# Kernel tuning notes

Hardware: AMD Instinct MI355X
Metric: run time of the kernel (lower is better)

Reference implementation:

```python
import jax, jax.numpy as jnp
import numpy as np

B, T, D = 1, 2048, 2048
N_HEADS, N_KV = 32, 8
HD = D // N_HEADS          # 64
G = N_HEADS // N_KV        # 4 query heads per kv head


def setup_inputs() -> dict:
    key = jax.random.key(0)
    ks = jax.random.split(key, 8)
    x = jax.random.normal(ks[0], (B, T, D), dtype=jnp.float32)
    cos = jax.random.uniform(ks[1], (1, 1, T, HD), dtype=jnp.float32)
    sin = jax.random.uniform(ks[2], (1, 1, T, HD), dtype=jnp.float32)
    attention_mask = jnp.ones((B, T), dtype=jnp.int32)
    s = 1.0 / np.sqrt(D)
    Wq = jax.random.normal(ks[3], (D, D), dtype=jnp.float32) * s
    Wk = jax.random.normal(ks[4], (D, N_KV * HD), dtype=jnp.float32) * s
    Wv = jax.random.normal(ks[5], (D, N_KV * HD), dtype=jnp.float32) * s
    Wo = jax.random.normal(ks[6], (D, D), dtype=jnp.float32) * s
    return {"x": x, "cos": cos, "sin": sin, "attention_mask": attention_mask,
            "Wq": Wq, "Wk": Wk, "Wv": Wv, "Wo": Wo}


def rotate_half(t):
    t1, t2 = jnp.split(t, 2, axis=-1)
    return jnp.concatenate((-t2, t1), axis=-1)


def reference(x, cos, sin, attention_mask, Wq, Wk, Wv, Wo):
    b, t, d = x.shape
    # projections (Linear, no bias); weights stored as [in, out]
    q = (x @ Wq).reshape(b, t, N_HEADS, HD).transpose(0, 2, 1, 3)   # [B,H,T,hd]
    k = (x @ Wk).reshape(b, t, N_KV, HD).transpose(0, 2, 1, 3)      # [B,Kv,T,hd]
    v = (x @ Wv).reshape(b, t, N_KV, HD).transpose(0, 2, 1, 3)      # [B,Kv,T,hd]
    # RoPE
    q = q * cos + rotate_half(q) * sin
    k = k * cos + rotate_half(k) * sin
    # GQA without materializing repeated KV: group query heads by kv head
    qg = q.reshape(b, N_KV, G, t, HD)                               # [B,Kv,G,T,hd]
    scale = 1.0 / jnp.sqrt(jnp.asarray(HD, dtype=x.dtype))
    scores = jnp.einsum('bkgqd,bkcd->bkgqc', qg, k) * scale          # [B,Kv,G,T,T]
    neg = jnp.finfo(x.dtype).min
    # padding mask: (1 - mask) * finfo.min, broadcast over heads/query pos
    pad = (1.0 - attention_mask.astype(x.dtype)) * neg               # [B,T]
    scores = scores + pad[:, None, None, None, :]
    # causal mask
    causal = jnp.tril(jnp.ones((t, t), dtype=bool))
    scores = jnp.where(causal[None, None, None, :, :], scores, neg)
    p = jax.nn.softmax(scores, axis=-1)
    y = jnp.einsum('bkgqc,bkcd->bkgqd', p, v)                        # [B,Kv,G,T,hd]
    y = y.reshape(b, N_HEADS, t, HD).transpose(0, 2, 1, 3).reshape(b, t, d)
    return y @ Wo
```

## Files before the change

### kernel.cpp

```cpp
#include <hip/hip_runtime.h>
#include <hip/hip_bf16.h>
#include <math.h>

typedef __attribute__((ext_vector_type(4))) float f32x4;
typedef __attribute__((ext_vector_type(8))) short bf16x8;
typedef __attribute__((ext_vector_type(4))) short bf16x4;
typedef unsigned short u16;
typedef unsigned int u32;


__device__ __forceinline__ float exp2fast(float x) {
    return __builtin_amdgcn_exp2f(x);
}
__device__ __forceinline__ u16 f2bf(float f) {
    return __builtin_bit_cast(u16, __float2bfloat16(f));
}
__device__ __forceinline__ float bf2f(u16 h) {
    return __builtin_bit_cast(float, ((u32)h) << 16);
}

#define GLL16(gsrc, ldst) __builtin_amdgcn_global_load_lds( \
    (const __attribute__((address_space(1))) u32*)(gsrc),   \
    (__attribute__((address_space(3))) u32*)(ldst), 16, 0, 0)

__device__ __forceinline__ void tconv_body(const float* __restrict__ in, u16* __restrict__ out,
                                           int R, int C, int bx, int by,
                                           float (*tile)[33], int tx, int ty) {
    int c0 = bx * 32, r0 = by * 32;
    #pragma unroll
    for (int i = 0; i < 4; ++i)
        tile[ty + i * 8][tx] = in[(size_t)(r0 + ty + i * 8) * C + c0 + tx];
    __syncthreads();
    #pragma unroll
    for (int i = 0; i < 4; ++i)
        out[(size_t)(c0 + ty + i * 8) * R + r0 + tx] = f2bf(tile[tx][ty + i * 8]);
}

__global__ void k_prep(const float* __restrict__ x, u16* __restrict__ xb,
                       const float* __restrict__ Wq, const float* __restrict__ Wk,
                       const float* __restrict__ Wv, const float* __restrict__ Wo,
                       u16* __restrict__ Wt, u16* __restrict__ WoT) {
    __shared__ float tile[32][33];
    const int r = blockIdx.x;
    const int tx = threadIdx.x, ty = threadIdx.y;
    if (r < 4096) {
        int tid = ty * 32 + tx;
        int base = (r * 256 + tid) * 4;
        float4 v = *(const float4*)(x + base);
        ushort4 o;
        o.x = f2bf(v.x); o.y = f2bf(v.y); o.z = f2bf(v.z); o.w = f2bf(v.w);
        *(ushort4*)(xb + base) = o;
    } else if (r < 8192) {
        int rr = r - 4096;  tconv_body(Wq, Wt, 2048, 2048, rr & 63, rr >> 6, tile, tx, ty);
    } else if (r < 9216) {
        int rr = r - 8192;  tconv_body(Wk, Wt + (size_t)2048 * 2048, 2048, 512, rr & 15, rr >> 4, tile, tx, ty);
    } else if (r < 10240) {
        int rr = r - 9216;  tconv_body(Wv, Wt + (size_t)2560 * 2048, 2048, 512, rr & 15, rr >> 4, tile, tx, ty);
    } else {
        int rr = r - 10240; tconv_body(Wo, WoT, 2048, 2048, rr & 63, rr >> 6, tile, tx, ty);
    }
}

__global__ void k_vprep(const u16* __restrict__ QKV,
                        const int* __restrict__ maskp, float* __restrict__ padf,
                        u16* __restrict__ Vt, int* __restrict__ padAny) {
    __shared__ u16 tile[32][34];
    const int r = blockIdx.x;
    const int tx = threadIdx.x, ty = threadIdx.y;
    if (r < 1024) {
        int c0 = (r & 15) * 32, r0 = (r >> 4) * 32;
        const u16* in = QKV + 2560;
        #pragma unroll
        for (int i = 0; i < 4; ++i)
            tile[ty + i * 8][tx] = in[(size_t)(r0 + ty + i * 8) * 3072 + c0 + tx];
        __syncthreads();
        int kv = r0 + tx;
        int kvp = (kv & ~63) + (((kv >> 5) & 1) << 5) + (((kv >> 2) & 3) << 3)
                + (((kv >> 4) & 1) << 2) + (kv & 3);
        #pragma unroll
        for (int i = 0; i < 4; ++i)
            Vt[(size_t)(c0 + ty + i * 8) * 2048 + kvp] = tile[tx][ty + i * 8];
    } else if (r < 1032) {
        int tid = ty * 32 + tx;
        int t = (r - 1024) * 256 + tid;
        padf[t] = maskp[t] ? 0.0f : -3.4028235e38f;
    } else {
        int t64 = r - 1032;
        int tid = ty * 32 + tx;
        if (tid < 64) {
            bool anypad = (maskp[t64 * 64 + tid] == 0);
            unsigned long long b = __ballot(anypad);
            if (tid == 0) padAny[t64] = (b != 0ULL) ? 1 : 0;
        }
    }
}

template<int OUTF32, int ROPE>
__global__ __launch_bounds__(256) void k_gemm(const u16* __restrict__ A, int lda,
                                              const u16* __restrict__ Bt,
                                              void* __restrict__ Cv,
                                              int M, int N, int K,
                                              const float* __restrict__ cosp,
                                              const float* __restrict__ sinp) {
    __shared__ u16 As[2][64 * 64];
    __shared__ u16 Bs[2][128 * 64];
    const int tid = threadIdx.x;
    const int w = tid >> 6, lane = tid & 63;
    const int wr = w & 1, wc = w >> 1;
    const int g = lane >> 4, l15 = lane & 15;
    const int m0 = blockIdx.y * 64, n0 = blockIdx.x * 128;

    f32x4 acc[2][4] = {};

    const u16* gA[2];
    const u16* gB[4];
    #pragma unroll
    for (int i = 0; i < 2; ++i) {
        int c = tid + i * 256;
        int rr = c >> 3, kc = (c & 7) ^ (rr & 7);
        gA[i] = A + (size_t)(m0 + rr) * lda + kc * 8;
    }
    #pragma unroll
    for (int i = 0; i < 4; ++i) {
        int c = tid + i * 256;
        int rr = c >> 3, kc = (c & 7) ^ (rr & 7);
        gB[i] = Bt + (size_t)(n0 + rr) * K + kc * 8;
    }

    auto stageAB = [&](int b, int k0) {
        #pragma unroll
        for (int i = 0; i < 2; ++i)
            GLL16(gA[i] + k0, &As[b][(tid + i * 256) * 8]);
        #pragma unroll
        for (int i = 0; i < 4; ++i)
            GLL16(gB[i] + k0, &Bs[b][(tid + i * 256) * 8]);
    };

    stageAB(0, 0);
    __syncthreads();
    int buf = 0;

    for (int k0 = 0; k0 < K; k0 += 64) {
        int kn = k0 + 64;
        if (kn < K) stageAB(buf ^ 1, kn);

        bf16x8 af[2][2], bfr[4][2];
        #pragma unroll
        for (int mt = 0; mt < 2; ++mt) {
            int row = wr * 32 + mt * 16 + l15;
            int rb = row * 64;
            #pragma unroll
            for (int kk = 0; kk < 2; ++kk) {
                int slot = (kk * 4 + g) ^ (row & 7);
                af[mt][kk] = *(const bf16x8*)&As[buf][rb + slot * 8];
            }
        }
        #pragma unroll
        for (int nt = 0; nt < 4; ++nt) {
            int row = wc * 64 + nt * 16 + l15;
            int rb = row * 64;
            #pragma unroll
            for (int kk = 0; kk < 2; ++kk) {
                int slot = (kk * 4 + g) ^ (row & 7);
                bfr[nt][kk] = *(const bf16x8*)&Bs[buf][rb + slot * 8];
            }
        }
        #pragma unroll
        for (int mt = 0; mt < 2; ++mt)
            #pragma unroll
            for (int nt = 0; nt < 4; ++nt) {
                acc[mt][nt] = __builtin_amdgcn_mfma_f32_16x16x32_bf16(af[mt][0], bfr[nt][0], acc[mt][nt], 0, 0, 0);
                acc[mt][nt] = __builtin_amdgcn_mfma_f32_16x16x32_bf16(af[mt][1], bfr[nt][1], acc[mt][nt], 0, 0, 0);
            }
        __syncthreads();
        buf ^= 1;
    }

    if (ROPE && n0 < 2560) {
        const float sc = (n0 < 2048) ? 0.18033688f : 1.0f;
        #pragma unroll
        for (int mt = 0; mt < 2; ++mt) {
            #pragma unroll
            for (int rr = 0; rr < 4; ++rr) {
                int t = m0 + wr * 32 + mt * 16 + g * 4 + rr;
                #pragma unroll
                for (int nt = 0; nt < 2; ++nt) {
                    int jh = nt * 16 + l15;
                    float c1 = cosp[t * 64 + jh],      s1 = sinp[t * 64 + jh];
                    float c2 = cosp[t * 64 + jh + 32], s2 = sinp[t * 64 + jh + 32];
                    float a = acc[mt][nt][rr], b = acc[mt][nt + 2][rr];
                    acc[mt][nt][rr]     = (a * c1 - b * s1) * sc;
                    acc[mt][nt + 2][rr] = (b * c2 + a * s2) * sc;
                }
            }
        }
    }

    #pragma unroll
    for (int mt = 0; mt < 2; ++mt) {
        #pragma unroll
        for (int nt = 0; nt < 4; ++nt) {
            int mrow = m0 + wr * 32 + mt * 16 + g * 4;
            int ncol = n0 + wc * 64 + nt * 16 + l15;
            #pragma unroll
            for (int rr = 0; rr < 4; ++rr) {
                float v = acc[mt][nt][rr];
                if (OUTF32) ((float*)Cv)[(size_t)(mrow + rr) * N + ncol] = v;
                else        ((u16*)Cv)[(size_t)(mrow + rr) * N + ncol] = f2bf(v);
            }
        }
    }
}

__global__ __launch_bounds__(512) void k_attn(const u16* __restrict__ QKV,
                                              const u16* __restrict__ VtG,
                                              const float* __restrict__ padf,
                                              const int* __restrict__ padAny,
                                              u16* __restrict__ Ob) {
    __shared__ u16 Ks[2][64 * 64];
    __shared__ u16 Vs[2][64 * 64];
    const int kvh = blockIdx.y;
    const int x = (int)blockIdx.x;
    const int tid = threadIdx.x;
    const int w = tid >> 6, lane = tid & 63;
    const int g = lane >> 4, l15 = lane & 15;
    const int h = kvh * 4 + (w & 3);
    const int q0w = (w >> 2) == 0 ? x * 16 : (127 - x) * 16;
    const int q = q0w + l15;
    const int myfull = q0w >> 6;
    const int iters = (((127 - x) * 16) >> 6) + 1;
    const bf16x8 ones8 = {(short)0x3F80, (short)0x3F80, (short)0x3F80, (short)0x3F80,
                          (short)0x3F80, (short)0x3F80, (short)0x3F80, (short)0x3F80};

    const u16* qrow = QKV + (size_t)q * 3072 + h * 64;
    bf16x8 qf0 = *(const bf16x8*)(qrow + g * 8);
    bf16x8 qf1 = *(const bf16x8*)(qrow + 32 + g * 8);

    f32x4 oacc[4] = {};
    float m_run = -1e30f, l_run = 0.0f;

    auto stage = [&](int b, int kv0) {
        int p = tid;
        int rr = p >> 3, c = p & 7;
        int cs = c ^ (rr & 7);
        GLL16(QKV + (size_t)(kv0 + rr) * 3072 + 2048 + kvh * 64 + cs * 8, &Ks[b][p * 8]);
        GLL16(VtG + (size_t)(kvh * 64 + rr) * 2048 + kv0 + cs * 8, &Vs[b][p * 8]);
    };

    stage(0, 0);
    __syncthreads();
    int buf = 0;

    for (int t = 0; t < iters; ++t) {
        const int kv0 = t * 64;
        if (t + 1 < iters) stage(buf ^ 1, kv0 + 64);

        if (t <= myfull) {
            const bool masked = (t == myfull);

            f32x4 st[4];
            __builtin_amdgcn_s_setprio(1);
            #pragma unroll
            for (int j = 0; j < 4; ++j) {
                int row = j * 16 + l15;
                int rb = row * 64, sw = (row & 7) << 3;
                bf16x8 kf0 = *(const bf16x8*)&Ks[buf][rb + ((g << 3) ^ sw)];
                bf16x8 kf1 = *(const bf16x8*)&Ks[buf][rb + ((32 + (g << 3)) ^ sw)];
                f32x4 z = {};
                st[j] = __builtin_amdgcn_mfma_f32_16x16x32_bf16(kf0, qf0, z, 0, 0, 0);
                st[j] = __builtin_amdgcn_mfma_f32_16x16x32_bf16(kf1, qf1, st[j], 0, 0, 0);
            }
            __builtin_amdgcn_s_setprio(0);

            float s[4][4];
            if (padAny[t]) {
                #pragma unroll
                for (int j = 0; j < 4; ++j) {
                    f32x4 pd = *(const f32x4*)(padf + kv0 + j * 16 + g * 4);
                    #pragma unroll
                    for (int rr = 0; rr < 4; ++rr) s[j][rr] = st[j][rr] + pd[rr];
                }
            } else {
                #pragma unroll
                for (int j = 0; j < 4; ++j)
                    #pragma unroll
                    for (int rr = 0; rr < 4; ++rr) s[j][rr] = st[j][rr];
            }
            if (masked) {
                #pragma unroll
                for (int j = 0; j < 4; ++j)
                    #pragma unroll
                    for (int rr = 0; rr < 4; ++rr) {
                        int kv = kv0 + j * 16 + g * 4 + rr;
                        if (kv > q) s[j][rr] = -INFINITY;
                    }
            }
            float m01 = fmaxf(fmaxf(s[0][0], s[0][1]), fmaxf(s[0][2], s[0][3]));
            float m23 = fmaxf(fmaxf(s[1][0], s[1][1]), fmaxf(s[1][2], s[1][3]));
            float m45 = fmaxf(fmaxf(s[2][0], s[2][1]), fmaxf(s[2][2], s[2][3]));
            float m67 = fmaxf(fmaxf(s[3][0], s[3][1]), fmaxf(s[3][2], s[3][3]));
            float tm = fmaxf(fmaxf(m01, m23), fmaxf(m45, m67));
            tm = fmaxf(tm, __shfl_xor(tm, 16));
            tm = fmaxf(tm, __shfl_xor(tm, 32));
            if (__any(tm > m_run + 11.5f)) {
                float m_new = fmaxf(m_run, tm);
                float fac = exp2fast(m_run - m_new);
                #pragma unroll
                for (int dt = 0; dt < 4; ++dt) oacc[dt] *= fac;
                l_run *= fac;
                m_run = m_new;
            }
            bf16x4 pb[4];
            #pragma unroll
            for (int j = 0; j < 4; ++j)
                #pragma unroll
                for (int rr = 0; rr < 4; ++rr)
                    pb[j][rr] = (short)f2bf(exp2fast(s[j][rr] - m_run));
            bf16x8 pbp0 = {pb[0][0], pb[0][1], pb[0][2], pb[0][3],
                           pb[1][0], pb[1][1], pb[1][2], pb[1][3]};
            bf16x8 pbp1 = {pb[2][0], pb[2][1], pb[2][2], pb[2][3],
                           pb[3][0], pb[3][1], pb[3][2], pb[3][3]};

            __builtin_amdgcn_s_setprio(1);
            {
                f32x4 la = {};
                la = __builtin_amdgcn_mfma_f32_16x16x32_bf16(ones8, pbp0, la, 0, 0, 0);
                la = __builtin_amdgcn_mfma_f32_16x16x32_bf16(ones8, pbp1, la, 0, 0, 0);
                l_run += la[0];
            }
            #pragma unroll
            for (int dt = 0; dt < 4; ++dt) {
                int row = dt * 16 + l15;
                int rb = row * 64, sw7 = row & 7;
                bf16x8 v0 = *(const bf16x8*)&Vs[buf][rb + ((g ^ sw7) << 3)];
                bf16x8 v1 = *(const bf16x8*)&Vs[buf][rb + (((4 + g) ^ sw7) << 3)];
                oacc[dt] = __builtin_amdgcn_mfma_f32_16x16x32_bf16(v0, pbp0, oacc[dt], 0, 0, 0);
                oacc[dt] = __builtin_amdgcn_mfma_f32_16x16x32_bf16(v1, pbp1, oacc[dt], 0, 0, 0);
            }
            __builtin_amdgcn_s_setprio(0);
        }
        __syncthreads();
        buf ^= 1;
    }

    float il = 1.0f / l_run;
    u16* orow = Ob + (size_t)q * 3072 + h * 64;
    #pragma unroll
    for (int dt = 0; dt < 4; ++dt) {
        ushort4 o;
        o.x = f2bf(oacc[dt][0] * il);
        o.y = f2bf(oacc[dt][1] * il);
        o.z = f2bf(oacc[dt][2] * il);
        o.w = f2bf(oacc[dt][3] * il);
        *(ushort4*)(orow + dt * 16 + g * 4) = o;
    }
}

extern "C" void kernel_launch(void* const* d_in, const int* in_sizes, int n_in,
                              void* d_out, int out_size, void* d_ws, size_t ws_size,
                              hipStream_t stream) {
    const float* x    = (const float*)d_in[0];
    const float* cosp = (const float*)d_in[1];
    const float* sinp = (const float*)d_in[2];
    const int*   mask = (const int*)d_in[3];
    const float* Wq   = (const float*)d_in[4];
    const float* Wk   = (const float*)d_in[5];
    const float* Wv   = (const float*)d_in[6];
    const float* Wo   = (const float*)d_in[7];
    float* out = (float*)d_out;

    char* ws = (char*)d_ws;
    u16* xb  = (u16*)ws; ws += (size_t)2048 * 2048 * 2;
    u16* Wt  = (u16*)ws; ws += (size_t)3072 * 2048 * 2;
    u16* WoT = (u16*)ws; ws += (size_t)2048 * 2048 * 2;
    u16* QKV = (u16*)ws; ws += (size_t)2048 * 3072 * 2;
    u16* Vt  = (u16*)ws; ws += (size_t)512 * 2048 * 2;
    float* padf = (float*)ws; ws += 2048 * 4;
    int* padAny = (int*)ws;

    dim3 tb(32, 8);
    k_prep<<<14336, tb, 0, stream>>>(x, xb, Wq, Wk, Wv, Wo, Wt, WoT);

    k_gemm<0, 1><<<dim3(24, 32), 256, 0, stream>>>(xb, 2048, Wt, QKV, 2048, 3072, 2048, cosp, sinp);

    k_vprep<<<1064, tb, 0, stream>>>(QKV, mask, padf, Vt, padAny);

    k_attn<<<dim3(64, 8), 512, 0, stream>>>(QKV, Vt, padf, padAny, QKV);

    k_gemm<1, 0><<<dim3(16, 32), 256, 0, stream>>>(QKV, 3072, WoT, out, 2048, 2048, 2048, nullptr, nullptr);
}
```

Measured before the change: 126.7 us.

## Fuse V transpose into QKV GEMM and fold mask prep into prep kernel

Removes the separate k_vprep kernel. The QKV GEMM now also computes V^T directly: extra blocks swap the A/B operands (Wv^T times x^T) and write the transposed, permuted Vt layout, so QKV shrinks to 2560 columns. Mask/padAny preparation moves into k_prep. This saves one kernel launch and the V read-transpose-write round trip. In exchange, the Vt stores from the GEMM epilogue are scattered 2-byte writes, and the padAny loop is serial per thread.

```diff
diff --git a/kernel.cpp b/kernel.cpp
--- a/kernel.cpp
+++ b/kernel.cpp
@@ -39,7 +39,9 @@
 __global__ void k_prep(const float* __restrict__ x, u16* __restrict__ xb,
                        const float* __restrict__ Wq, const float* __restrict__ Wk,
                        const float* __restrict__ Wv, const float* __restrict__ Wo,
-                       u16* __restrict__ Wt, u16* __restrict__ WoT) {
+                       u16* __restrict__ Wt, u16* __restrict__ WoT,
+                       const int* __restrict__ maskp, float* __restrict__ padf,
+                       int* __restrict__ padAny) {
     __shared__ float tile[32][33];
     const int r = blockIdx.x;
     const int tx = threadIdx.x, ty = threadIdx.y;
@@ -56,50 +58,27 @@
         int rr = r - 8192;  tconv_body(Wk, Wt + (size_t)2048 * 2048, 2048, 512, rr & 15, rr >> 4, tile, tx, ty);
     } else if (r < 10240) {
         int rr = r - 9216;  tconv_body(Wv, Wt + (size_t)2560 * 2048, 2048, 512, rr & 15, rr >> 4, tile, tx, ty);
-    } else {
+    } else if (r < 14336) {
         int rr = r - 10240; tconv_body(Wo, WoT, 2048, 2048, rr & 63, rr >> 6, tile, tx, ty);
-    }
-}
-
-__global__ void k_vprep(const u16* __restrict__ QKV,
-                        const int* __restrict__ maskp, float* __restrict__ padf,
-                        u16* __restrict__ Vt, int* __restrict__ padAny) {
-    __shared__ u16 tile[32][34];
-    const int r = blockIdx.x;
-    const int tx = threadIdx.x, ty = threadIdx.y;
-    if (r < 1024) {
-        int c0 = (r & 15) * 32, r0 = (r >> 4) * 32;
-        const u16* in = QKV + 2560;
-        #pragma unroll
-        for (int i = 0; i < 4; ++i)
-            tile[ty + i * 8][tx] = in[(size_t)(r0 + ty + i * 8) * 3072 + c0 + tx];
-        __syncthreads();
-        int kv = r0 + tx;
-        int kvp = (kv & ~63) + (((kv >> 5) & 1) << 5) + (((kv >> 2) & 3) << 3)
-                + (((kv >> 4) & 1) << 2) + (kv & 3);
-        #pragma unroll
-        for (int i = 0; i < 4; ++i)
-            Vt[(size_t)(c0 + ty + i * 8) * 2048 + kvp] = tile[tx][ty + i * 8];
-    } else if (r < 1032) {
+    } else if (r < 14344) {
         int tid = ty * 32 + tx;
-        int t = (r - 1024) * 256 + tid;
+        int t = (r - 14336) * 256 + tid;
         padf[t] = maskp[t] ? 0.0f : -3.4028235e38f;
     } else {
-        int t64 = r - 1032;
         int tid = ty * 32 + tx;
-        if (tid < 64) {
-            bool anypad = (maskp[t64 * 64 + tid] == 0);
-            unsigned long long b = __ballot(anypad);
-            if (tid == 0) padAny[t64] = (b != 0ULL) ? 1 : 0;
-        }
-    }
-}
-
-template<int OUTF32, int ROPE>
-__global__ __launch_bounds__(256) void k_gemm(const u16* __restrict__ A, int lda,
-                                              const u16* __restrict__ Bt,
+        if (tid < 32) {
+            int any = 0;
+            for (int i = 0; i < 64; ++i) any |= (maskp[tid * 64 + i] == 0);
+            padAny[tid] = any;
+        }
+    }
+}
+
+template<int MODE>
+__global__ __launch_bounds__(256) void k_gemm(const u16* __restrict__ A0,
+                                              const u16* __restrict__ B0,
                                               void* __restrict__ Cv,
-                                              int M, int N, int K,
+                                              u16* __restrict__ Vt,
                                               const float* __restrict__ cosp,
                                               const float* __restrict__ sinp) {
     __shared__ u16 As[2][64 * 64];
@@ -108,7 +87,20 @@
     const int w = tid >> 6, lane = tid & 63;
     const int wr = w & 1, wc = w >> 1;
     const int g = lane >> 4, l15 = lane & 15;
-    const int m0 = blockIdx.y * 64, n0 = blockIdx.x * 128;
+    const int K = 2048;
+
+    int m0, n0, lda;
+    const u16 *Ap, *Btp;
+    bool isVT = false;
+    if (MODE == 1) {
+        int bid = blockIdx.x;
+        isVT = (bid >= 640);
+        if (!isVT) { m0 = (bid / 20) * 64; n0 = (bid % 20) * 128; Ap = A0; lda = 2048; Btp = B0; }
+        else { int vb = bid - 640; m0 = (vb & 7) * 64; n0 = (vb >> 3) * 128;
+               Ap = B0 + (size_t)2560 * 2048; lda = 2048; Btp = A0; }
+    } else {
+        m0 = blockIdx.y * 64; n0 = blockIdx.x * 128; Ap = A0; lda = 2560; Btp = B0;
+    }
 
     f32x4 acc[2][4] = {};
 
@@ -118,13 +110,13 @@
     for (int i = 0; i < 2; ++i) {
         int c = tid + i * 256;
         int rr = c >> 3, kc = (c & 7) ^ (rr & 7);
-        gA[i] = A + (size_t)(m0 + rr) * lda + kc * 8;
+        gA[i] = Ap + (size_t)(m0 + rr) * lda + kc * 8;
     }
     #pragma unroll
     for (int i = 0; i < 4; ++i) {
         int c = tid + i * 256;
         int rr = c >> 3, kc = (c & 7) ^ (rr & 7);
-        gB[i] = Bt + (size_t)(n0 + rr) * K + kc * 8;
+        gB[i] = Btp + (size_t)(n0 + rr) * K + kc * 8;
     }
 
     auto stageAB = [&](int b, int k0) {
@@ -176,7 +168,7 @@
         buf ^= 1;
     }
 
-    if (ROPE && n0 < 2560) {
+    if (MODE == 1 && !isVT) {
         const float sc = (n0 < 2048) ? 0.18033688f : 1.0f;
         #pragma unroll
         for (int mt = 0; mt < 2; ++mt) {
@@ -205,8 +197,16 @@
             #pragma unroll
             for (int rr = 0; rr < 4; ++rr) {
                 float v = acc[mt][nt][rr];
-                if (OUTF32) ((float*)Cv)[(size_t)(mrow + rr) * N + ncol] = v;
-                else        ((u16*)Cv)[(size_t)(mrow + rr) * N + ncol] = f2bf(v);
+                if (MODE == 0) {
+                    ((float*)Cv)[(size_t)(mrow + rr) * 2048 + ncol] = v;
+                } else if (!isVT) {
+                    ((u16*)Cv)[(size_t)(mrow + rr) * 2560 + ncol] = f2bf(v);
+                } else {
+                    int t = ncol;
+                    int kvp = (t & ~63) | (((t >> 5) & 1) << 5) | (((t >> 2) & 3) << 3)
+                            | (((t >> 4) & 1) << 2) | (t & 3);
+                    Vt[(size_t)(mrow + rr) * 2048 + kvp] = f2bf(v);
+                }
             }
         }
     }
@@ -232,7 +232,7 @@
     const bf16x8 ones8 = {(short)0x3F80, (short)0x3F80, (short)0x3F80, (short)0x3F80,
                           (short)0x3F80, (short)0x3F80, (short)0x3F80, (short)0x3F80};
 
-    const u16* qrow = QKV + (size_t)q * 3072 + h * 64;
+    const u16* qrow = QKV + (size_t)q * 2560 + h * 64;
     bf16x8 qf0 = *(const bf16x8*)(qrow + g * 8);
     bf16x8 qf1 = *(const bf16x8*)(qrow + 32 + g * 8);
 
@@ -243,7 +243,7 @@
         int p = tid;
         int rr = p >> 3, c = p & 7;
         int cs = c ^ (rr & 7);
-        GLL16(QKV + (size_t)(kv0 + rr) * 3072 + 2048 + kvh * 64 + cs * 8, &Ks[b][p * 8]);
+        GLL16(QKV + (size_t)(kv0 + rr) * 2560 + 2048 + kvh * 64 + cs * 8, &Ks[b][p * 8]);
         GLL16(VtG + (size_t)(kvh * 64 + rr) * 2048 + kv0 + cs * 8, &Vs[b][p * 8]);
     };
 
@@ -344,7 +344,7 @@
     }
 
     float il = 1.0f / l_run;
-    u16* orow = Ob + (size_t)q * 3072 + h * 64;
+    u16* orow = Ob + (size_t)q * 2560 + h * 64;
     #pragma unroll
     for (int dt = 0; dt < 4; ++dt) {
         ushort4 o;
@@ -373,19 +373,17 @@
     u16* xb  = (u16*)ws; ws += (size_t)2048 * 2048 * 2;
     u16* Wt  = (u16*)ws; ws += (size_t)3072 * 2048 * 2;
     u16* WoT = (u16*)ws; ws += (size_t)2048 * 2048 * 2;
-    u16* QKV = (u16*)ws; ws += (size_t)2048 * 3072 * 2;
+    u16* QKV = (u16*)ws; ws += (size_t)2048 * 2560 * 2;
     u16* Vt  = (u16*)ws; ws += (size_t)512 * 2048 * 2;
     float* padf = (float*)ws; ws += 2048 * 4;
     int* padAny = (int*)ws;
 
     dim3 tb(32, 8);
-    k_prep<<<14336, tb, 0, stream>>>(x, xb, Wq, Wk, Wv, Wo, Wt, WoT);
-
-    k_gemm<0, 1><<<dim3(24, 32), 256, 0, stream>>>(xb, 2048, Wt, QKV, 2048, 3072, 2048, cosp, sinp);
-
-    k_vprep<<<1064, tb, 0, stream>>>(QKV, mask, padf, Vt, padAny);
+    k_prep<<<14345, tb, 0, stream>>>(x, xb, Wq, Wk, Wv, Wo, Wt, WoT, mask, padf, padAny);
+
+    k_gemm<1><<<768, 256, 0, stream>>>(xb, Wt, QKV, Vt, cosp, sinp);
 
     k_attn<<<dim3(64, 8), 512, 0, stream>>>(QKV, Vt, padf, padAny, QKV);
 
-    k_gemm<1, 0><<<dim3(16, 32), 256, 0, stream>>>(QKV, 3072, WoT, out, 2048, 2048, 2048, nullptr, nullptr);
-}
+    k_gemm<0><<<dim3(16, 32), 256, 0, stream>>>(QKV, WoT, out, nullptr, nullptr, nullptr);
+}
```

After: 130.4 us. 1.03x slower.
